# Kernel tuning notes

Measured on AMD Instinct MI355X. Metric: run time of the kernel, lower is better.

## Reference

```python
import jax, jax.numpy as jnp
import numpy as np

V = 32000   # target_vocab_size
E = 512     # embedding_dim
L = 2       # enc_lstm_layers
HD = 512    # enc_lstm_hidden_dim (bidirectional encoder)
H = 2 * HD  # decoder LSTM hidden size
B = 16
T = 128
BOS = 1
CTX = L * 2 * HD          # stepwise context dim = 2048
IN0 = E + CTX             # decoder LSTM layer-0 input dim = 2560


def setup_inputs() -> dict:
    key = jax.random.key(0)
    ks = jax.random.split(key, 12)
    def w(k, shape, fan_in):
        return jax.random.normal(k, shape, jnp.float32) * np.float32(1.0 / np.sqrt(fan_in))
    return {
        "enc_lstm_hidden": jax.random.normal(ks[0], (2 * L, B, HD), jnp.float32),
        "enc_lstm_ctxt": jax.random.normal(ks[1], (2 * L, B, HD), jnp.float32),
        "minibatch_target": jax.random.randint(ks[2], (B, T), 0, V, dtype=jnp.int32),
        "emb": w(ks[3], (V, E), E),
        "w_ih_0": w(ks[4], (4 * H, IN0), IN0),
        "w_hh_0": w(ks[5], (4 * H, H), H),
        "b_ih_0": jnp.zeros((4 * H,), jnp.float32),
        "b_hh_0": jnp.zeros((4 * H,), jnp.float32),
        "w_ih_1": w(ks[6], (4 * H, H), H),
        "w_hh_1": w(ks[7], (4 * H, H), H),
        "b_ih_1": jnp.zeros((4 * H,), jnp.float32),
        "b_hh_1": jnp.zeros((4 * H,), jnp.float32),
        "fc_w": w(ks[8], (V, H), H),
        "fc_b": jnp.zeros((V,), jnp.float32),
    }


def _lstm_layer(x_seq, h0, c0, w_ih, w_hh, b):
    """x_seq: [T, B, in]; returns top outputs [T, B, H]. torch gate order i,f,g,o."""
    def step(carry, x):
        h, c = carry
        g = x @ w_ih.T + h @ w_hh.T + b
        i, f, gg, o = jnp.split(g, 4, axis=-1)
        c = jax.nn.sigmoid(f) * c + jax.nn.sigmoid(i) * jnp.tanh(gg)
        h = jax.nn.sigmoid(o) * jnp.tanh(c)
        return (h, c), h
    (hT, cT), ys = jax.lax.scan(step, (h0, c0), x_seq)
    return ys, hT, cT


def reference(enc_lstm_hidden, enc_lstm_ctxt, minibatch_target, emb,
              w_ih_0, w_hh_0, b_ih_0, b_hh_0,
              w_ih_1, w_hh_1, b_ih_1, b_hh_1, fc_w, fc_b):
    # _reshape_encoder_state: [2L,B,HD] -> [L,B,2HD] (interleave fwd/bwd per layer)
    def reshape_state(s):
        return s.reshape(L, 2, B, HD).transpose(0, 2, 1, 3).reshape(L, B, 2 * HD)
    h0 = reshape_state(enc_lstm_hidden)
    c0 = reshape_state(enc_lstm_ctxt)
    # stepwise input context: [B, 2L*HD]
    ctx = jnp.transpose(enc_lstm_hidden, (1, 0, 2)).reshape(B, CTX)
    # teacher forcing: prev tokens = [BOS, target[:, :-1]]
    tokens = jnp.concatenate(
        [jnp.full((B, 1), BOS, minibatch_target.dtype), minibatch_target[:, :-1]], axis=1)
    tok_emb = emb[tokens]                                   # [B,T,E]
    ctx_b = jnp.broadcast_to(ctx[:, None, :], (B, T, CTX))  # [B,T,CTX]
    x = jnp.concatenate([tok_emb, ctx_b], axis=-1).transpose(1, 0, 2)  # [T,B,IN0]
    x, _, _ = _lstm_layer(x, h0[0], c0[0], w_ih_0, w_hh_0, b_ih_0 + b_hh_0)
    x, _, _ = _lstm_layer(x, h0[1], c0[1], w_ih_1, w_hh_1, b_ih_1 + b_hh_1)
    out = jnp.tanh(x)                                       # [T,B,H]
    logits = jnp.einsum('tbh,vh->btv', out, fc_w) + fc_b    # [B,T,V]
    return logits
```

## Files before the change

### kernel.cpp

```cpp
#include <hip/hip_runtime.h>


#define NBLK 256

typedef float f32x4 __attribute__((ext_vector_type(4)));
typedef __bf16 bf16x8 __attribute__((ext_vector_type(8)));
typedef unsigned short u16;

__device__ __forceinline__ float sigf(float x) { return 1.0f / (1.0f + __expf(-x)); }
__device__ __forceinline__ float tanh_(float x) {
  x = fminf(15.0f, fmaxf(-15.0f, x));
  float e = __expf(2.0f * x);
  return (e - 1.0f) / (e + 1.0f);
}

__device__ __forceinline__ u16 f2bf(float f) {
  __bf16 h = (__bf16)f;
  return __builtin_bit_cast(u16, h);
}

__device__ __forceinline__ bf16x8 cvt8(float4 a, float4 b) {
  bf16x8 v;
  v[0] = (__bf16)a.x; v[1] = (__bf16)a.y; v[2] = (__bf16)a.z; v[3] = (__bf16)a.w;
  v[4] = (__bf16)b.x; v[5] = (__bf16)b.y; v[6] = (__bf16)b.z; v[7] = (__bf16)b.w;
  return v;
}

__device__ __forceinline__ void st_cv16(u16* p, u16 v) {
  unsigned vv = v;
  asm volatile("global_store_short %0, %1, off sc0 sc1" :: "v"(p), "v"(vv) : "memory");
}

__device__ __forceinline__ void flag_store(unsigned* p, unsigned v) {
  asm volatile(
      "s_waitcnt vmcnt(0)\n\t"
      "global_store_dword %0, %1, off sc0 sc1"
      :: "v"(p), "v"(v) : "memory");
}

__device__ __forceinline__ void ld4_flags(const unsigned* p, unsigned& a, unsigned& b,
                                          unsigned& c, unsigned& d) {
  asm volatile(
      "global_load_dword %0, %4, off sc0 sc1\n\t"
      "global_load_dword %1, %5, off sc0 sc1\n\t"
      "global_load_dword %2, %6, off sc0 sc1\n\t"
      "global_load_dword %3, %7, off sc0 sc1\n\t"
      "s_waitcnt vmcnt(0)"
      : "=&v"(a), "=&v"(b), "=&v"(c), "=&v"(d)
      : "v"(p), "v"(p + 16), "v"(p + 32), "v"(p + 48)
      : "memory");
}

__device__ __forceinline__ void gsyncf(unsigned step, unsigned* bar) {
  __syncthreads();
  const int tid = threadIdx.x;
  if (tid == 0) flag_store(bar + 16 + blockIdx.x * 16, step);
  if (tid < 64) {
    const unsigned* base = bar + 16 + tid * 64;
    for (;;) {
      unsigned a, b, c, d;
      ld4_flags(base, a, b, c, d);
      bool mine = (a >= step) & (b >= step) & (c >= step) & (d >= step);
      if (__all(mine)) break;
      __builtin_amdgcn_s_sleep(1);
    }
    asm volatile("" ::: "memory");
  }
  __syncthreads();
}

__device__ __forceinline__ void dot4(float& a, float4 wv, float4 xv) {
  a = fmaf(wv.x, xv.x, a);
  a = fmaf(wv.y, xv.y, a);
  a = fmaf(wv.z, xv.z, a);
  a = fmaf(wv.w, xv.w, a);
}

__global__ void prep_emb(const int* __restrict__ tgt, const float* __restrict__ emb,
                         u16* __restrict__ x0b) {
  const int g = blockIdx.x * blockDim.x + threadIdx.x;
  const int col8 = (g & 63) * 8;
  const int tb = g >> 6;
  const int t = tb >> 4, b = tb & 15;
  const int tok = (t == 0) ? 1 : tgt[b * 128 + (t - 1)];
  const float* s = emb + (size_t)tok * 512 + col8;
  float4 a = *(const float4*)s;
  float4 bb = *(const float4*)(s + 4);
  __align__(16) u16 r[8] = {f2bf(a.x), f2bf(a.y), f2bf(a.z), f2bf(a.w),
                            f2bf(bb.x), f2bf(bb.y), f2bf(bb.z), f2bf(bb.w)};
  *(uint4*)(x0b + (size_t)tb * 512 + col8) = *(uint4*)r;
}

__global__ __launch_bounds__(256, 1) void prep_ctx(const float* __restrict__ enc_h,
                                                   const float* __restrict__ wih0,
                                                   float* __restrict__ cp) {
  __shared__ float ctx[16][2052];
  const int tid = threadIdx.x;
#pragma unroll
  for (int c = 0; c < 32; ++c) {
    int f4 = tid + c * 256;
    int b = f4 >> 9, kq = f4 & 511;
    *(float4*)&ctx[b][kq * 4] =
        *(const float4*)(enc_h + (kq >> 7) * 8192 + b * 512 + (kq & 127) * 4);
  }
  __syncthreads();
  const int jr = tid >> 4, b = tid & 15;
  const int j = blockIdx.x * 16 + jr;
  const float* w = wih0 + (size_t)j * 2560 + 512;
  float a0 = 0.f, a1 = 0.f, a2 = 0.f, a3 = 0.f;
  for (int k = 0; k < 2048; k += 16) {
    float4 w0 = *(const float4*)(w + k);
    float4 w1 = *(const float4*)(w + k + 4);
    float4 w2 = *(const float4*)(w + k + 8);
    float4 w3 = *(const float4*)(w + k + 12);
    float4 x0 = *(const float4*)&ctx[b][k];
    float4 x1 = *(const float4*)&ctx[b][k + 4];
    float4 x2 = *(const float4*)&ctx[b][k + 8];
    float4 x3 = *(const float4*)&ctx[b][k + 12];
    dot4(a0, w0, x0); dot4(a1, w1, x1); dot4(a2, w2, x2); dot4(a3, w3, x3);
  }
  cp[(size_t)j * 16 + b] = a0 + a1 + a2 + a3;
}

#define BURST(ACC, BP, S, XOFF)                                              \
  _Pragma("unroll")                                                          \
  for (int mm = 0; mm < 16; ++mm) {                                          \
    bf16x8 av = *(const bf16x8*)&(BP)[fr * (S) + (XOFF) + mm * 32 + ks8];    \
    ACC = __builtin_amdgcn_mfma_f32_16x16x32_bf16(av, bw[mm], ACC, 0, 0, 0); \
  }

__global__ __launch_bounds__(512, 1) void dec_seq_rw(
    const float* __restrict__ enc_h, const float* __restrict__ enc_c,
    const float* __restrict__ wih0, const float* __restrict__ whh0,
    const float* __restrict__ wih1, const float* __restrict__ whh1,
    const float* __restrict__ bih0, const float* __restrict__ bhh0,
    const float* __restrict__ bih1, const float* __restrict__ bhh1,
    const float* __restrict__ cp, const u16* __restrict__ x0b,
    u16* __restrict__ xr, u16* __restrict__ h1r,
    u16* __restrict__ out2b, unsigned* bar) {
  __shared__ u16 xe[16 * 520];
  __shared__ u16 xs[16 * 1032];
  __shared__ u16 h1s[16 * 1032];
  __shared__ float gls[7][16][17];

  const int tid = threadIdx.x;
  const int wgid = blockIdx.x;
  const int w4 = wgid * 4;
  const int lane = tid & 63;
  const int wave = tid >> 6;
  const int fr = lane & 15;
  const int ks8 = (lane >> 4) * 8;
  unsigned step = 0;

  bf16x8 bw[16];
  {
    const int nn = lane & 15;
    const int j = (nn >> 2) * 1024 + w4 + (nn & 3);
    const float* wsrc = nullptr;
    size_t wstride = 1024;
    int wko = 0;
    if (wave == 0) { wsrc = wih0; wstride = 2560; wko = 0; }
    else if (wave == 1) { wsrc = whh0; wko = 0; }
    else if (wave == 2) { wsrc = whh0; wko = 512; }
    else if (wave == 3) { wsrc = wih1; wko = 0; }
    else if (wave == 4) { wsrc = wih1; wko = 512; }
    else if (wave == 5) { wsrc = whh1; wko = 0; }
    else if (wave == 6) { wsrc = whh1; wko = 512; }
    if (wsrc) {
      const float* base = wsrc + (size_t)j * wstride + wko + (lane >> 4) * 8;
#pragma unroll
      for (int mm = 0; mm < 16; ++mm) {
        const float* sp = base + mm * 32;
        bw[mm] = cvt8(*(const float4*)sp, *(const float4*)(sp + 4));
      }
    } else {
#pragma unroll
      for (int mm = 0; mm < 16; ++mm) bw[mm] = bf16x8{};
    }
  }

  const int gdj = tid >> 4;
  const int gb = tid & 15;
  float cpA0 = 0.f, cpA1 = 0.f, cpA2 = 0.f, cpA3 = 0.f;
  float cpB0 = 0.f, cpB1 = 0.f, cpB2 = 0.f, cpB3 = 0.f;
  float c0r = 0.f, c1r = 0.f;
  if (tid < 64) {
    const int jp = w4 + gdj;
    cpA0 = cp[(size_t)(jp) * 16 + gb] + bih0[jp] + bhh0[jp];
    cpA1 = cp[(size_t)(1024 + jp) * 16 + gb] + bih0[1024 + jp] + bhh0[1024 + jp];
    cpA2 = cp[(size_t)(2048 + jp) * 16 + gb] + bih0[2048 + jp] + bhh0[2048 + jp];
    cpA3 = cp[(size_t)(3072 + jp) * 16 + gb] + bih0[3072 + jp] + bhh0[3072 + jp];
    cpB0 = bih1[jp] + bhh1[jp];
    cpB1 = bih1[1024 + jp] + bhh1[1024 + jp];
    cpB2 = bih1[2048 + jp] + bhh1[2048 + jp];
    cpB3 = bih1[3072 + jp] + bhh1[3072 + jp];
    const int dir = jp >> 9, e = jp & 511;
    c0r = enc_c[dir * 8192 + gb * 512 + e];
    c1r = enc_c[(2 + dir) * 8192 + gb * 512 + e];
    st_cv16(xr + gb * 1024 + jp, f2bf(enc_h[dir * 8192 + gb * 512 + e]));
    st_cv16(h1r + gb * 1024 + jp, f2bf(enc_h[(2 + dir) * 8192 + gb * 512 + e]));
  }
  gsyncf(++step, bar);

  const int sm = tid >> 5;
  const int skq = (tid & 31) * 8;

  for (int s = 0; s < 129; ++s) {
    const bool doA = (s < 128), doB = (s >= 1);

    uint4 rx[4], rh[4] = {}, re[2] = {};
    {
      const u16* sx = xr + (size_t)s * 16384 + sm * 1024;
#pragma unroll
      for (int jj = 0; jj < 4; ++jj) rx[jj] = *(const uint4*)(sx + skq + jj * 256);
      if (doB) {
        const u16* sh = h1r + (size_t)(s - 1) * 16384 + sm * 1024;
#pragma unroll
        for (int jj = 0; jj < 4; ++jj) rh[jj] = *(const uint4*)(sh + skq + jj * 256);
      }
      if (doA) {
        const u16* se = x0b + (size_t)s * 8192 + sm * 512;
#pragma unroll
        for (int jj = 0; jj < 2; ++jj) re[jj] = *(const uint4*)(se + skq + jj * 256);
      }
    }
#pragma unroll
    for (int jj = 0; jj < 4; ++jj) *(uint4*)&xs[sm * 1032 + skq + jj * 256] = rx[jj];
    if (doB) {
#pragma unroll
      for (int jj = 0; jj < 4; ++jj) *(uint4*)&h1s[sm * 1032 + skq + jj * 256] = rh[jj];
    }
    if (doA) {
#pragma unroll
      for (int jj = 0; jj < 2; ++jj) *(uint4*)&xe[sm * 520 + skq + jj * 256] = re[jj];
    }
    __syncthreads();

    f32x4 acc = {0.f, 0.f, 0.f, 0.f};
    bool act = false;
    if (wave == 0) { if (doA) { BURST(acc, xe, 520, 0) act = true; } }
    else if (wave == 1) { if (doA) { BURST(acc, xs, 1032, 0) act = true; } }
    else if (wave == 2) { if (doA) { BURST(acc, xs, 1032, 512) act = true; } }
    else if (wave == 3) { if (doB) { BURST(acc, xs, 1032, 0) act = true; } }
    else if (wave == 4) { if (doB) { BURST(acc, xs, 1032, 512) act = true; } }
    else if (wave == 5) { if (doB) { BURST(acc, h1s, 1032, 0) act = true; } }
    else if (wave == 6) { if (doB) { BURST(acc, h1s, 1032, 512) act = true; } }
    if (act) {
#pragma unroll
      for (int r = 0; r < 4; ++r) gls[wave][fr][(lane >> 4) * 4 + r] = acc[r];
    }
    __syncthreads();

    if (tid < 64) {
      const int jp = w4 + gdj;
      if (doA) {
        float gi = gls[0][gdj][gb] + gls[1][gdj][gb] + gls[2][gdj][gb] + cpA0;
        float gf = gls[0][4 + gdj][gb] + gls[1][4 + gdj][gb] + gls[2][4 + gdj][gb] + cpA1;
        float gg = gls[0][8 + gdj][gb] + gls[1][8 + gdj][gb] + gls[2][8 + gdj][gb] + cpA2;
        float go = gls[0][12 + gdj][gb] + gls[1][12 + gdj][gb] + gls[2][12 + gdj][gb] + cpA3;
        c0r = sigf(gf) * c0r + sigf(gi) * tanh_(gg);
        float h = sigf(go) * tanh_(c0r);
        st_cv16(xr + (size_t)(s + 1) * 16384 + gb * 1024 + jp, f2bf(h));
      }
      if (doB) {
        float gi = gls[3][gdj][gb] + gls[4][gdj][gb] + gls[5][gdj][gb] +
                   gls[6][gdj][gb] + cpB0;
        float gf = gls[3][4 + gdj][gb] + gls[4][4 + gdj][gb] + gls[5][4 + gdj][gb] +
                   gls[6][4 + gdj][gb] + cpB1;
        float gg = gls[3][8 + gdj][gb] + gls[4][8 + gdj][gb] + gls[5][8 + gdj][gb] +
                   gls[6][8 + gdj][gb] + cpB2;
        float go = gls[3][12 + gdj][gb] + gls[4][12 + gdj][gb] + gls[5][12 + gdj][gb] +
                   gls[6][12 + gdj][gb] + cpB3;
        c1r = sigf(gf) * c1r + sigf(gi) * tanh_(gg);
        float h = sigf(go) * tanh_(c1r);
        st_cv16(h1r + (size_t)s * 16384 + gb * 1024 + jp, f2bf(h));
        out2b[((s - 1) * 16 + gb) * 1024 + jp] = f2bf(tanh_(h));
      }
    }
    gsyncf(++step, bar);
  }
}

__global__ __launch_bounds__(256, 2) void fc_gemm_mfma(
    const u16* __restrict__ A, const float* __restrict__ Bw,
    const float* __restrict__ bias, float* __restrict__ C) {
  __shared__ __align__(16) u16 Al[128][40];
  __shared__ __align__(16) u16 Bl[128][40];

  const int tid = threadIdx.x;
  const int m0 = blockIdx.x * 128;
  const int n0 = blockIdx.y * 128;
  const int wave = tid >> 6;
  const int lane = tid & 63;
  const int wm = (wave & 1) * 64;
  const int wn = (wave >> 1) * 64;
  const int fr = lane & 15;
  const int ks = lane >> 4;

  const int srow = tid >> 1;
  const int sh16 = (tid & 1) * 16;

  const u16* Ag = A + (size_t)(m0 + srow) * 1024 + sh16;
  const float* Bg = Bw + (size_t)(n0 + srow) * 1024 + sh16;

  f32x4 acc[4][4] = {};

  for (int k0 = 0; k0 < 1024; k0 += 32) {
    uint4 a0 = *(const uint4*)(Ag + k0);
    uint4 a1 = *(const uint4*)(Ag + k0 + 8);
    float bfv[16];
    *(float4*)&bfv[0] = *(const float4*)(Bg + k0);
    *(float4*)&bfv[4] = *(const float4*)(Bg + k0 + 4);
    *(float4*)&bfv[8] = *(const float4*)(Bg + k0 + 8);
    *(float4*)&bfv[12] = *(const float4*)(Bg + k0 + 12);
    u16 bu[16];
#pragma unroll
    for (int u = 0; u < 16; ++u) bu[u] = f2bf(bfv[u]);

    __syncthreads();
    *(uint4*)&Al[srow][sh16] = a0;
    *(uint4*)&Al[srow][sh16 + 8] = a1;
    *(uint4*)&Bl[srow][sh16] = *(uint4*)&bu[0];
    *(uint4*)&Bl[srow][sh16 + 8] = *(uint4*)&bu[8];
    __syncthreads();

    bf16x8 af[4], bf[4];
#pragma unroll
    for (int i = 0; i < 4; ++i) af[i] = *(const bf16x8*)&Al[wm + i * 16 + fr][ks * 8];
#pragma unroll
    for (int j = 0; j < 4; ++j) bf[j] = *(const bf16x8*)&Bl[wn + j * 16 + fr][ks * 8];
#pragma unroll
    for (int i = 0; i < 4; ++i)
#pragma unroll
      for (int j = 0; j < 4; ++j)
        acc[i][j] = __builtin_amdgcn_mfma_f32_16x16x32_bf16(af[i], bf[j], acc[i][j], 0, 0, 0);
  }

  float bj[4];
#pragma unroll
  for (int j = 0; j < 4; ++j) bj[j] = bias[n0 + wn + j * 16 + fr];

  const int mrb = (lane >> 4) * 4;
#pragma unroll
  for (int i = 0; i < 4; ++i) {
#pragma unroll
    for (int r = 0; r < 4; ++r) {
      const int m = m0 + wm + i * 16 + mrb + r;
      float* dst = C + ((size_t)(m & 15) * 128 + (m >> 4)) * 32000;
#pragma unroll
      for (int j = 0; j < 4; ++j) {
        dst[n0 + wn + j * 16 + fr] = acc[i][j][r] + bj[j];
      }
    }
  }
}

extern "C" void kernel_launch(void* const* d_in, const int* in_sizes, int n_in,
                              void* d_out, int out_size, void* d_ws, size_t ws_size,
                              hipStream_t stream) {
  const float* enc_h = (const float*)d_in[0];
  const float* enc_c = (const float*)d_in[1];
  const int* tgt = (const int*)d_in[2];
  const float* emb = (const float*)d_in[3];
  const float* wih0 = (const float*)d_in[4];
  const float* whh0 = (const float*)d_in[5];
  const float* bih0 = (const float*)d_in[6];
  const float* bhh0 = (const float*)d_in[7];
  const float* wih1 = (const float*)d_in[8];
  const float* whh1 = (const float*)d_in[9];
  const float* bih1 = (const float*)d_in[10];
  const float* bhh1 = (const float*)d_in[11];
  const float* fcw = (const float*)d_in[12];
  const float* fcb = (const float*)d_in[13];
  float* logits = (float*)d_out;

  unsigned* bar = (unsigned*)d_ws;
  hipMemsetAsync(d_ws, 0, 64 + 256 * 64, stream);

  float* cp = (float*)((char*)d_ws + 32768);
  u16* x0b = (u16*)(cp + 65536);
  u16* xr = x0b + 1048576;
  u16* h1r = xr + 2113536;
  u16* out2b = h1r + 2113536;

  prep_emb<<<512, 256, 0, stream>>>(tgt, emb, x0b);
  prep_ctx<<<256, 256, 0, stream>>>(enc_h, wih0, cp);
  dec_seq_rw<<<NBLK, 512, 0, stream>>>(enc_h, enc_c, wih0, whh0, wih1, whh1,
                                       bih0, bhh0, bih1, bhh1, cp, x0b,
                                       xr, h1r, out2b, bar);
  fc_gemm_mfma<<<dim3(16, 250), 256, 0, stream>>>(out2b, fcw, fcb, logits);
}
```

Baseline: 1.081 ms.

## Halve persistent decoder blocks, each owning eight hidden units with two weight tiles per wave

The persistent recurrent kernel now runs on 128 workgroups instead of 256. Each workgroup handles 8 hidden units, and each wave holds two register-resident bf16 weight tiles, issuing two MFMA bursts per step. Fewer participants cut the cost of the grid-wide flag barrier, which now polls two flags per lane instead of four. The embedding tile for the next step is prefetched into shared memory after the MFMA phase. The trade is more serial MFMA work per wave and higher register pressure per block.

```diff
diff --git a/kernel.cpp b/kernel.cpp
--- a/kernel.cpp
+++ b/kernel.cpp
@@ -1,7 +1,7 @@
 #include <hip/hip_runtime.h>
 
 
-#define NBLK 256
+#define NBLK 128
 
 typedef float f32x4 __attribute__((ext_vector_type(4)));
 typedef __bf16 bf16x8 __attribute__((ext_vector_type(8)));
@@ -32,36 +32,32 @@
 }
 
 __device__ __forceinline__ void flag_store(unsigned* p, unsigned v) {
+  asm volatile("global_store_dword %0, %1, off sc0 sc1" :: "v"(p), "v"(v) : "memory");
+}
+
+__device__ __forceinline__ void ld2_flags(const unsigned* p0, const unsigned* p1,
+                                          unsigned& a, unsigned& b) {
   asm volatile(
-      "s_waitcnt vmcnt(0)\n\t"
-      "global_store_dword %0, %1, off sc0 sc1"
-      :: "v"(p), "v"(v) : "memory");
-}
-
-__device__ __forceinline__ void ld4_flags(const unsigned* p, unsigned& a, unsigned& b,
-                                          unsigned& c, unsigned& d) {
-  asm volatile(
-      "global_load_dword %0, %4, off sc0 sc1\n\t"
-      "global_load_dword %1, %5, off sc0 sc1\n\t"
-      "global_load_dword %2, %6, off sc0 sc1\n\t"
-      "global_load_dword %3, %7, off sc0 sc1\n\t"
+      "global_load_dword %0, %2, off sc0 sc1\n\t"
+      "global_load_dword %1, %3, off sc0 sc1\n\t"
       "s_waitcnt vmcnt(0)"
-      : "=&v"(a), "=&v"(b), "=&v"(c), "=&v"(d)
-      : "v"(p), "v"(p + 16), "v"(p + 32), "v"(p + 48)
+      : "=&v"(a), "=&v"(b)
+      : "v"(p0), "v"(p1)
       : "memory");
 }
 
 __device__ __forceinline__ void gsyncf(unsigned step, unsigned* bar) {
+  asm volatile("s_waitcnt vmcnt(0)" ::: "memory");
   __syncthreads();
   const int tid = threadIdx.x;
-  if (tid == 0) flag_store(bar + 16 + blockIdx.x * 16, step);
+  if (tid == 0) flag_store(bar + 32 + blockIdx.x * 32, step);
   if (tid < 64) {
-    const unsigned* base = bar + 16 + tid * 64;
+    const unsigned* p0 = bar + 32 + tid * 64;
+    const unsigned* p1 = p0 + 32;
     for (;;) {
-      unsigned a, b, c, d;
-      ld4_flags(base, a, b, c, d);
-      bool mine = (a >= step) & (b >= step) & (c >= step) & (d >= step);
-      if (__all(mine)) break;
+      unsigned a, b;
+      ld2_flags(p0, p1, a, b);
+      if (__all((a >= step) & (b >= step))) break;
       __builtin_amdgcn_s_sleep(1);
     }
     asm volatile("" ::: "memory");
@@ -122,14 +118,37 @@
   cp[(size_t)j * 16 + b] = a0 + a1 + a2 + a3;
 }
 
-#define BURST(ACC, BP, S, XOFF)                                              \
-  _Pragma("unroll")                                                          \
-  for (int mm = 0; mm < 16; ++mm) {                                          \
-    bf16x8 av = *(const bf16x8*)&(BP)[fr * (S) + (XOFF) + mm * 32 + ks8];    \
-    ACC = __builtin_amdgcn_mfma_f32_16x16x32_bf16(av, bw[mm], ACC, 0, 0, 0); \
-  }
-
-__global__ __launch_bounds__(512, 1) void dec_seq_rw(
+#define BURST(ACC, BP, S, XOFF, BW)                                            \
+  _Pragma("unroll")                                                            \
+  for (int mm = 0; mm < 16; ++mm) {                                            \
+    bf16x8 av = *(const bf16x8*)&(BP)[fr * (S) + (XOFF) + mm * 32 + ks8];      \
+    ACC = __builtin_amdgcn_mfma_f32_16x16x32_bf16(av, (BW)[mm], ACC, 0, 0, 0); \
+  }
+
+__device__ __forceinline__ void loadw(bf16x8* dst, int q, int w8, int lane,
+                                      const float* wih0, const float* whh0,
+                                      const float* wih1, const float* whh1) {
+  const int c = q >> 1, tile = q & 1;
+  const int nn = lane & 15;
+  const int gate = tile * 2 + (nn >> 3);
+  const int unit = nn & 7;
+  const int j = gate * 1024 + w8 + unit;
+  const float* src;
+  size_t stride = 1024;
+  int ko = 0;
+  if (c == 0) { src = wih0; stride = 2560; ko = 0; }
+  else if (c <= 2) { src = whh0; ko = (c - 1) * 512; }
+  else if (c <= 4) { src = wih1; ko = (c - 3) * 512; }
+  else { src = whh1; ko = (c - 5) * 512; }
+  const float* base = src + (size_t)j * stride + ko + ((lane >> 4) * 8);
+#pragma unroll
+  for (int mm = 0; mm < 16; ++mm) {
+    const float* sp = base + mm * 32;
+    dst[mm] = cvt8(*(const float4*)sp, *(const float4*)(sp + 4));
+  }
+}
+
+__global__ __launch_bounds__(512, 2) void dec_seq_rw2(
     const float* __restrict__ enc_h, const float* __restrict__ enc_c,
     const float* __restrict__ wih0, const float* __restrict__ whh0,
     const float* __restrict__ wih1, const float* __restrict__ whh1,
@@ -141,51 +160,33 @@
   __shared__ u16 xe[16 * 520];
   __shared__ u16 xs[16 * 1032];
   __shared__ u16 h1s[16 * 1032];
-  __shared__ float gls[7][16][17];
+  __shared__ float gls[14][16][17];
 
   const int tid = threadIdx.x;
   const int wgid = blockIdx.x;
-  const int w4 = wgid * 4;
+  const int w8 = wgid * 8;
   const int lane = tid & 63;
   const int wave = tid >> 6;
   const int fr = lane & 15;
   const int ks8 = (lane >> 4) * 8;
   unsigned step = 0;
 
-  bf16x8 bw[16];
-  {
-    const int nn = lane & 15;
-    const int j = (nn >> 2) * 1024 + w4 + (nn & 3);
-    const float* wsrc = nullptr;
-    size_t wstride = 1024;
-    int wko = 0;
-    if (wave == 0) { wsrc = wih0; wstride = 2560; wko = 0; }
-    else if (wave == 1) { wsrc = whh0; wko = 0; }
-    else if (wave == 2) { wsrc = whh0; wko = 512; }
-    else if (wave == 3) { wsrc = wih1; wko = 0; }
-    else if (wave == 4) { wsrc = wih1; wko = 512; }
-    else if (wave == 5) { wsrc = whh1; wko = 0; }
-    else if (wave == 6) { wsrc = whh1; wko = 512; }
-    if (wsrc) {
-      const float* base = wsrc + (size_t)j * wstride + wko + (lane >> 4) * 8;
-#pragma unroll
-      for (int mm = 0; mm < 16; ++mm) {
-        const float* sp = base + mm * 32;
-        bw[mm] = cvt8(*(const float4*)sp, *(const float4*)(sp + 4));
-      }
-    } else {
-#pragma unroll
-      for (int mm = 0; mm < 16; ++mm) bw[mm] = bf16x8{};
-    }
-  }
-
-  const int gdj = tid >> 4;
+  bf16x8 bw0[16], bw1[16];
+  const int q0 = (wave < 6) ? 2 * wave : (wave == 6 ? 12 : 13);
+  loadw(bw0, q0, w8, lane, wih0, whh0, wih1, whh1);
+  if (wave < 6) loadw(bw1, 2 * wave + 1, w8, lane, wih0, whh0, wih1, whh1);
+  else {
+#pragma unroll
+    for (int mm = 0; mm < 16; ++mm) bw1[mm] = bf16x8{};
+  }
+
+  const int gdj = (tid >> 4) & 7;
   const int gb = tid & 15;
   float cpA0 = 0.f, cpA1 = 0.f, cpA2 = 0.f, cpA3 = 0.f;
   float cpB0 = 0.f, cpB1 = 0.f, cpB2 = 0.f, cpB3 = 0.f;
   float c0r = 0.f, c1r = 0.f;
-  if (tid < 64) {
-    const int jp = w4 + gdj;
+  if (tid < 128) {
+    const int jp = w8 + gdj;
     cpA0 = cp[(size_t)(jp) * 16 + gb] + bih0[jp] + bhh0[jp];
     cpA1 = cp[(size_t)(1024 + jp) * 16 + gb] + bih0[1024 + jp] + bhh0[1024 + jp];
     cpA2 = cp[(size_t)(2048 + jp) * 16 + gb] + bih0[2048 + jp] + bhh0[2048 + jp];
@@ -200,10 +201,17 @@
     st_cv16(xr + gb * 1024 + jp, f2bf(enc_h[dir * 8192 + gb * 512 + e]));
     st_cv16(h1r + gb * 1024 + jp, f2bf(enc_h[(2 + dir) * 8192 + gb * 512 + e]));
   }
-  gsyncf(++step, bar);
 
   const int sm = tid >> 5;
   const int skq = (tid & 31) * 8;
+
+  {
+    const u16* se = x0b + sm * 512;
+#pragma unroll
+    for (int jj = 0; jj < 2; ++jj)
+      *(uint4*)&xe[sm * 520 + skq + jj * 256] = *(const uint4*)(se + skq + jj * 256);
+  }
+  gsyncf(++step, bar);
 
   for (int s = 0; s < 129; ++s) {
     const bool doA = (s < 128), doB = (s >= 1);
@@ -218,8 +226,8 @@
 #pragma unroll
         for (int jj = 0; jj < 4; ++jj) rh[jj] = *(const uint4*)(sh + skq + jj * 256);
       }
-      if (doA) {
-        const u16* se = x0b + (size_t)s * 8192 + sm * 512;
+      if (s < 127) {
+        const u16* se = x0b + (size_t)(s + 1) * 8192 + sm * 512;
 #pragma unroll
         for (int jj = 0; jj < 2; ++jj) re[jj] = *(const uint4*)(se + skq + jj * 256);
       }
@@ -230,47 +238,53 @@
 #pragma unroll
       for (int jj = 0; jj < 4; ++jj) *(uint4*)&h1s[sm * 1032 + skq + jj * 256] = rh[jj];
     }
-    if (doA) {
+    __syncthreads();
+
+    f32x4 acc0 = {0.f, 0.f, 0.f, 0.f}, acc1 = {0.f, 0.f, 0.f, 0.f};
+    bool act0 = false, act1 = false;
+    if (wave == 0) { if (doA) { BURST(acc0, xe, 520, 0, bw0) BURST(acc1, xe, 520, 0, bw1) act0 = act1 = true; } }
+    else if (wave == 1) { if (doA) { BURST(acc0, xs, 1032, 0, bw0) BURST(acc1, xs, 1032, 0, bw1) act0 = act1 = true; } }
+    else if (wave == 2) { if (doA) { BURST(acc0, xs, 1032, 512, bw0) BURST(acc1, xs, 1032, 512, bw1) act0 = act1 = true; } }
+    else if (wave == 3) { if (doB) { BURST(acc0, xs, 1032, 0, bw0) BURST(acc1, xs, 1032, 0, bw1) act0 = act1 = true; } }
+    else if (wave == 4) { if (doB) { BURST(acc0, xs, 1032, 512, bw0) BURST(acc1, xs, 1032, 512, bw1) act0 = act1 = true; } }
+    else if (wave == 5) { if (doB) { BURST(acc0, h1s, 1032, 0, bw0) BURST(acc1, h1s, 1032, 0, bw1) act0 = act1 = true; } }
+    else if (wave == 6) { if (doB) { BURST(acc0, h1s, 1032, 512, bw0) act0 = true; } }
+    else { if (doB) { BURST(acc0, h1s, 1032, 512, bw0) act0 = true; } }
+    if (act0) {
+#pragma unroll
+      for (int r = 0; r < 4; ++r) gls[q0][fr][(lane >> 4) * 4 + r] = acc0[r];
+    }
+    if (act1) {
+#pragma unroll
+      for (int r = 0; r < 4; ++r) gls[q0 + 1][fr][(lane >> 4) * 4 + r] = acc1[r];
+    }
+    __syncthreads();
+
+    if (s < 127) {
 #pragma unroll
       for (int jj = 0; jj < 2; ++jj) *(uint4*)&xe[sm * 520 + skq + jj * 256] = re[jj];
     }
-    __syncthreads();
-
-    f32x4 acc = {0.f, 0.f, 0.f, 0.f};
-    bool act = false;
-    if (wave == 0) { if (doA) { BURST(acc, xe, 520, 0) act = true; } }
-    else if (wave == 1) { if (doA) { BURST(acc, xs, 1032, 0) act = true; } }
-    else if (wave == 2) { if (doA) { BURST(acc, xs, 1032, 512) act = true; } }
-    else if (wave == 3) { if (doB) { BURST(acc, xs, 1032, 0) act = true; } }
-    else if (wave == 4) { if (doB) { BURST(acc, xs, 1032, 512) act = true; } }
-    else if (wave == 5) { if (doB) { BURST(acc, h1s, 1032, 0) act = true; } }
-    else if (wave == 6) { if (doB) { BURST(acc, h1s, 1032, 512) act = true; } }
-    if (act) {
-#pragma unroll
-      for (int r = 0; r < 4; ++r) gls[wave][fr][(lane >> 4) * 4 + r] = acc[r];
-    }
-    __syncthreads();
-
-    if (tid < 64) {
-      const int jp = w4 + gdj;
+
+    if (tid < 128) {
+      const int jp = w8 + gdj;
       if (doA) {
-        float gi = gls[0][gdj][gb] + gls[1][gdj][gb] + gls[2][gdj][gb] + cpA0;
-        float gf = gls[0][4 + gdj][gb] + gls[1][4 + gdj][gb] + gls[2][4 + gdj][gb] + cpA1;
-        float gg = gls[0][8 + gdj][gb] + gls[1][8 + gdj][gb] + gls[2][8 + gdj][gb] + cpA2;
-        float go = gls[0][12 + gdj][gb] + gls[1][12 + gdj][gb] + gls[2][12 + gdj][gb] + cpA3;
+        float gi = gls[0][gdj][gb] + gls[2][gdj][gb] + gls[4][gdj][gb] + cpA0;
+        float gf = gls[0][8 + gdj][gb] + gls[2][8 + gdj][gb] + gls[4][8 + gdj][gb] + cpA1;
+        float gg = gls[1][gdj][gb] + gls[3][gdj][gb] + gls[5][gdj][gb] + cpA2;
+        float go = gls[1][8 + gdj][gb] + gls[3][8 + gdj][gb] + gls[5][8 + gdj][gb] + cpA3;
         c0r = sigf(gf) * c0r + sigf(gi) * tanh_(gg);
         float h = sigf(go) * tanh_(c0r);
         st_cv16(xr + (size_t)(s + 1) * 16384 + gb * 1024 + jp, f2bf(h));
       }
       if (doB) {
-        float gi = gls[3][gdj][gb] + gls[4][gdj][gb] + gls[5][gdj][gb] +
-                   gls[6][gdj][gb] + cpB0;
-        float gf = gls[3][4 + gdj][gb] + gls[4][4 + gdj][gb] + gls[5][4 + gdj][gb] +
-                   gls[6][4 + gdj][gb] + cpB1;
-        float gg = gls[3][8 + gdj][gb] + gls[4][8 + gdj][gb] + gls[5][8 + gdj][gb] +
-                   gls[6][8 + gdj][gb] + cpB2;
-        float go = gls[3][12 + gdj][gb] + gls[4][12 + gdj][gb] + gls[5][12 + gdj][gb] +
-                   gls[6][12 + gdj][gb] + cpB3;
+        float gi = gls[6][gdj][gb] + gls[8][gdj][gb] + gls[10][gdj][gb] +
+                   gls[12][gdj][gb] + cpB0;
+        float gf = gls[6][8 + gdj][gb] + gls[8][8 + gdj][gb] + gls[10][8 + gdj][gb] +
+                   gls[12][8 + gdj][gb] + cpB1;
+        float gg = gls[7][gdj][gb] + gls[9][gdj][gb] + gls[11][gdj][gb] +
+                   gls[13][gdj][gb] + cpB2;
+        float go = gls[7][8 + gdj][gb] + gls[9][8 + gdj][gb] + gls[11][8 + gdj][gb] +
+                   gls[13][8 + gdj][gb] + cpB3;
         c1r = sigf(gf) * c1r + sigf(gi) * tanh_(gg);
         float h = sigf(go) * tanh_(c1r);
         st_cv16(h1r + (size_t)s * 16384 + gb * 1024 + jp, f2bf(h));
@@ -375,7 +389,7 @@
   float* logits = (float*)d_out;
 
   unsigned* bar = (unsigned*)d_ws;
-  hipMemsetAsync(d_ws, 0, 64 + 256 * 64, stream);
+  hipMemsetAsync(d_ws, 0, 32768, stream);
 
   float* cp = (float*)((char*)d_ws + 32768);
   u16* x0b = (u16*)(cp + 65536);
@@ -385,8 +399,8 @@
 
   prep_emb<<<512, 256, 0, stream>>>(tgt, emb, x0b);
   prep_ctx<<<256, 256, 0, stream>>>(enc_h, wih0, cp);
-  dec_seq_rw<<<NBLK, 512, 0, stream>>>(enc_h, enc_c, wih0, whh0, wih1, whh1,
-                                       bih0, bhh0, bih1, bhh1, cp, x0b,
-                                       xr, h1r, out2b, bar);
+  dec_seq_rw2<<<NBLK, 512, 0, stream>>>(enc_h, enc_c, wih0, whh0, wih1, whh1,
+                                        bih0, bhh0, bih1, bhh1, cp, x0b,
+                                        xr, h1r, out2b, bar);
   fc_gemm_mfma<<<dim3(16, 250), 256, 0, stream>>>(out2b, fcw, fcb, logits);
 }
```

Measured after the change: 1.048 ms. 1.03x faster.
